# Performance work log

Hardware: AMD Instinct MI355X
Metric: run time of the kernel (lower is better)

## Reference

```python
import jax, jax.numpy as jnp
import numpy as np
import math

B, S, D, H, L, D_OUT = 8, 1024, 1024, 16, 2, 1024
DK = D // H
LN_EPS = 1e-8


def _ln(x, g, b):
    m = jnp.mean(x, axis=-1, keepdims=True)
    var = jnp.mean((x - m) ** 2, axis=-1, keepdims=True)
    return (x - m) / jnp.sqrt(var + LN_EPS) * g + b


def setup_inputs() -> dict:
    key = jax.random.key(0)
    ks = jax.random.split(key, 16)
    s = 0.02
    return {
        "q": jax.random.normal(ks[0], (B, S, D), jnp.float32),
        "k": jax.random.normal(ks[1], (B, S, D), jnp.float32),
        "v": jax.random.normal(ks[2], (B, S, D), jnp.float32),
        "attn_mask": jnp.ones((B, S, S), jnp.int32),
        # per-layer stacked params
        "Wqkv": jax.random.normal(ks[3], (L, 3, D, D), jnp.float32) * s,  # [out,in]
        "bqkv": jnp.zeros((L, 3, D), jnp.float32),
        "Wo": jax.random.normal(ks[4], (L, D, D), jnp.float32) * s,
        "bo": jnp.zeros((L, D), jnp.float32),
        "ln1_g": jnp.ones((L, D), jnp.float32),
        "ln1_b": jnp.zeros((L, D), jnp.float32),
        "ln2_g": jnp.ones((L, D), jnp.float32),
        "ln2_b": jnp.zeros((L, D), jnp.float32),
        "Wc1": jax.random.normal(ks[5], (L, D, D), jnp.float32) * s,  # conv1d k=1 == linear
        "bc1": jnp.zeros((L, D), jnp.float32),
        "Wc2": jax.random.normal(ks[6], (L, D, D), jnp.float32) * s,
        "bc2": jnp.zeros((L, D), jnp.float32),
        "last_g": jnp.ones((D,), jnp.float32),
        "last_b": jnp.zeros((D,), jnp.float32),
        "Wfc": jax.random.normal(ks[7], (D_OUT, D), jnp.float32) * s,
        "bfc": jnp.zeros((D_OUT,), jnp.float32),
    }


def reference(q, k, v, attn_mask, Wqkv, bqkv, Wo, bo, ln1_g, ln1_b, ln2_g, ln2_b,
              Wc1, bc1, Wc2, bc2, last_g, last_b, Wfc, bfc):
    scale = 1.0 / math.sqrt(DK)
    mask = (attn_mask == 0)[:, None, :, :]  # [B,1,S,S] broadcast over heads

    def proj(x, W, b):
        # linear [out,in] then split heads -> [B,H,S,dk]
        y = jnp.einsum('bsd,od->bso', x, W) + b
        return y.reshape(B, S, H, DK).transpose(0, 2, 1, 3)

    for i in range(L):
        Q = _ln(q, ln1_g[i], ln1_b[i])
        qh = proj(Q, Wqkv[i, 0], bqkv[i, 0])
        kh = proj(k, Wqkv[i, 1], bqkv[i, 1])
        vh = proj(v, Wqkv[i, 2], bqkv[i, 2])
        scores = jnp.einsum('bhqd,bhkd->bhqk', qh, kh) * scale
        scores = jnp.clip(scores, -30.0, 30.0)
        scores = jnp.where(mask, -1e9, scores) + 1e-5
        p = jax.nn.softmax(scores, axis=-1)
        x = jnp.einsum('bhqk,bhkd->bhqd', p, vh)
        x = x.transpose(0, 2, 1, 3).reshape(B, S, D)
        x = jax.nn.relu(jnp.einsum('bsd,od->bso', x, Wo[i]) + bo[i])
        k = k + x
        k = _ln(k, ln2_g[i], ln2_b[i])
        # PointWiseFeedForward: conv2(conv1(x)) + x, kernel_size=1, no activation
        h = jnp.einsum('bsd,od->bso', k, Wc1[i]) + bc1[i]
        h = jnp.einsum('bsd,od->bso', h, Wc2[i]) + bc2[i]
        k = k + h
        q = k
        v = k
    out = _ln(k, last_g, last_b)
    return jnp.einsum('bsd,od->bso', out, Wfc) + bfc
```

## Files before the change

kernel.cpp:

```cpp
#include <hip/hip_runtime.h>

typedef __attribute__((ext_vector_type(8))) short s8x;
typedef __attribute__((ext_vector_type(4))) float f4x;
typedef unsigned short u16;
typedef unsigned int u32;

#define DEV static __device__ __forceinline__

DEV u16 f2b(float f) {
    union { float f; u32 u; } v; v.f = f;
    u32 r = v.u + 0x7FFFu + ((v.u >> 16) & 1u);
    return (u16)(r >> 16);
}

DEV u32 pk2(float lo, float hi) {
    u32 r;
    asm("v_cvt_pk_bf16_f32 %0, %1, %2" : "=v"(r) : "v"(lo), "v"(hi));
    return r;
}

DEV void gload16(const void* g, void* lds) {
    __builtin_amdgcn_global_load_lds(
        (const __attribute__((address_space(1))) void*)g,
        (__attribute__((address_space(3))) void*)lds, 16, 0, 0);
}

#define GK 1024
#define BM 128
#define BN 128
#define BK 64


DEV void stage_unit(const u16* __restrict__ g, char* l, int tid) {
#pragma unroll
    for (int i = 0; i < 2; ++i) {
        int db = i * 8192 + tid * 16;
        int row = db >> 7;
        int cs = ((db >> 4) & 7) ^ (row & 7);
        gload16(g + (size_t)row * 1024 + cs * 8, l + db);
    }
}

DEV s8x lds_frag(const char* Lbase, int row, int kk, int lg) {
    int cb = (kk * 64 + lg * 16) ^ ((row & 7) << 4);
    return *(const s8x*)(Lbase + row * 128 + cb);
}

template<int FLAGS, int NN>
__global__ __launch_bounds__(512, 2) void gemm8(
    const u16* __restrict__ A, const u16* __restrict__ W,
    const float* __restrict__ bias, const float* __restrict__ res,
    float* __restrict__ outf, u16* __restrict__ outb, float scl)
{
    constexpr bool RELU = (FLAGS & 1) != 0;
    constexpr bool RES  = (FLAGS & 2) != 0;
    constexpr bool WF   = (FLAGS & 4) != 0;
    constexpr bool WB   = (FLAGS & 8) != 0;
    constexpr bool RBIA = (FLAGS & 16) != 0;

    __shared__ __attribute__((aligned(16))) u16 As[3][256 * 64];
    __shared__ __attribute__((aligned(16))) u16 Bs[3][128 * 64];

    const int tid = threadIdx.x, lane = tid & 63, wid = tid >> 6;
    const int l15 = lane & 15, lg = lane >> 4;
    const int wm = wid >> 1, wn = wid & 1;
    const int bm = blockIdx.x, bn = blockIdx.y;

    const u16* Ab = A + (size_t)bm * 256 * GK;
    const u16* Wb = W + (size_t)bn * 128 * GK;

    f4x acc[4][4];
#pragma unroll
    for (int i = 0; i < 4; ++i)
#pragma unroll
        for (int j = 0; j < 4; ++j) { f4x z = {0.f, 0.f, 0.f, 0.f}; acc[i][j] = z; }

    char* a0 = (char*)As[0]; char* a1 = (char*)As[1]; char* a2 = (char*)As[2];
    char* b0 = (char*)Bs[0]; char* b1 = (char*)Bs[1]; char* b2 = (char*)Bs[2];

    stage_unit(Ab + 0 * 64,                 a0,        tid);
    stage_unit(Ab + 128 * GK + 0 * 64,      a0 + 16384, tid);
    stage_unit(Wb + 0 * 64,                 b0,        tid);
    stage_unit(Ab + 1 * 64,                 a1,        tid);
    stage_unit(Ab + 128 * GK + 1 * 64,      a1 + 16384, tid);
    stage_unit(Wb + 1 * 64,                 b1,        tid);
    asm volatile("s_waitcnt vmcnt(6)" ::: "memory");
    __builtin_amdgcn_s_barrier();

    for (int t = 0; t < 16; ++t) {
        const bool st = (t < 14);
        s8x bfr[4][2], afr[2][2];
#pragma unroll
        for (int ni = 0; ni < 4; ++ni)
#pragma unroll
            for (int kk = 0; kk < 2; ++kk)
                bfr[ni][kk] = lds_frag(b0, wn * 64 + ni * 16 + l15, kk, lg);
#pragma unroll
        for (int mi = 0; mi < 2; ++mi)
#pragma unroll
            for (int kk = 0; kk < 2; ++kk)
                afr[mi][kk] = lds_frag(a0, wm * 64 + mi * 16 + l15, kk, lg);
        if (st) {
            stage_unit(Ab + (t + 2) * 64,            a2,         tid);
            stage_unit(Ab + 128 * GK + (t + 2) * 64, a2 + 16384, tid);
        }
        __builtin_amdgcn_s_barrier();
        asm volatile("s_waitcnt lgkmcnt(0)" ::: "memory");
        __builtin_amdgcn_sched_barrier(0);
        __builtin_amdgcn_s_setprio(1);
#pragma unroll
        for (int kk = 0; kk < 2; ++kk)
#pragma unroll
            for (int mi = 0; mi < 2; ++mi)
#pragma unroll
                for (int ni = 0; ni < 4; ++ni)
                    acc[mi][ni] = __builtin_amdgcn_mfma_f32_16x16x32_bf16(afr[mi][kk], bfr[ni][kk], acc[mi][ni], 0, 0, 0);
        __builtin_amdgcn_s_setprio(0);
        __builtin_amdgcn_s_barrier();

        s8x afr2[2][2];
#pragma unroll
        for (int mi = 0; mi < 2; ++mi)
#pragma unroll
            for (int kk = 0; kk < 2; ++kk)
                afr2[mi][kk] = lds_frag(a0, wm * 64 + (mi + 2) * 16 + l15, kk, lg);
        if (st) stage_unit(Wb + (t + 2) * 64, b2, tid);
        __builtin_amdgcn_s_barrier();
        asm volatile("s_waitcnt lgkmcnt(0)" ::: "memory");
        __builtin_amdgcn_sched_barrier(0);
        __builtin_amdgcn_s_setprio(1);
#pragma unroll
        for (int kk = 0; kk < 2; ++kk)
#pragma unroll
            for (int mi = 0; mi < 2; ++mi)
#pragma unroll
                for (int ni = 0; ni < 4; ++ni)
                    acc[mi + 2][ni] = __builtin_amdgcn_mfma_f32_16x16x32_bf16(afr2[mi][kk], bfr[ni][kk], acc[mi + 2][ni], 0, 0, 0);
        __builtin_amdgcn_s_setprio(0);
        if (st) asm volatile("s_waitcnt vmcnt(6)" ::: "memory");
        else    asm volatile("s_waitcnt vmcnt(0)" ::: "memory");
        __builtin_amdgcn_s_barrier();

        char* tA = a0; a0 = a1; a1 = a2; a2 = tA;
        char* tB = b0; b0 = b1; b1 = b2; b2 = tB;
    }

#pragma unroll
    for (int ni = 0; ni < 4; ++ni) {
        int gcol = bn * 128 + wn * 64 + ni * 16 + l15;
        float bvc = RBIA ? 0.f : bias[gcol];
#pragma unroll
        for (int mi = 0; mi < 4; ++mi) {
            int grow0 = bm * 256 + wm * 64 + mi * 16 + lg * 4;
#pragma unroll
            for (int r = 0; r < 4; ++r) {
                float bv = RBIA ? bias[grow0 + r] : bvc;
                float v = (acc[mi][ni][r] + bv) * scl;
                if (RELU) v = fmaxf(v, 0.f);
                size_t oidx = (size_t)(grow0 + r) * NN + gcol;
                if (RES) v += res[oidx];
                if (WF) outf[oidx] = v;
                if (WB) outb[oidx] = f2b(v);
            }
        }
    }
}

__global__ __launch_bounds__(256) void gemm_z2(
    const u16* __restrict__ A0, const u16* __restrict__ W0, const float* __restrict__ b0,
    u16* __restrict__ o0, float s0,
    const u16* __restrict__ A1, const u16* __restrict__ W1, const float* __restrict__ b1,
    u16* __restrict__ o1, float s1)
{
    const int z = blockIdx.z;
    const u16* A = z ? A1 : A0;
    const u16* W = z ? W1 : W0;
    const float* bias = z ? b1 : b0;
    u16* outb = z ? o1 : o0;
    const float scl = z ? s1 : s0;

    __shared__ __attribute__((aligned(16))) u16 As[2][BM * BK];
    __shared__ __attribute__((aligned(16))) u16 Bs[2][BN * BK];

    const int tid  = threadIdx.x;
    const int lane = tid & 63;
    const int wid  = tid >> 6;
    const int wr = wid >> 1, wc = wid & 1;
    const int bm = blockIdx.x, bn = blockIdx.y;
    const int l15 = lane & 15;
    const int lg  = lane >> 4;

    const u16* Ab = A + (size_t)bm * BM * GK;
    const u16* Wb = W + (size_t)bn * BN * GK;

    const int prow = tid >> 3;
    const int pcol = (tid & 7) * 8;

    f4x acc[4][4];
#pragma unroll
    for (int i = 0; i < 4; ++i)
#pragma unroll
        for (int j = 0; j < 4; ++j) { f4x z_ = {0.f, 0.f, 0.f, 0.f}; acc[i][j] = z_; }

#pragma unroll
    for (int c = 0; c < 4; ++c) {
        int row = c * 32 + prow;
        gload16(Ab + (size_t)row * GK + pcol, &As[0][row * BK + pcol]);
    }
#pragma unroll
    for (int c = 0; c < 4; ++c) {
        int row = c * 32 + prow;
        gload16(Wb + (size_t)row * GK + pcol, &Bs[0][row * BK + pcol]);
    }

    const int nkt = GK / BK;
    int cur = 0;
    for (int kt = 0; kt < nkt; ++kt) {
        __syncthreads();
        if (kt + 1 < nkt) {
            const u16* Ak = Ab + (kt + 1) * BK;
            const u16* Wk = Wb + (kt + 1) * BK;
#pragma unroll
            for (int c = 0; c < 4; ++c) {
                int row = c * 32 + prow;
                gload16(Ak + (size_t)row * GK + pcol, &As[cur ^ 1][row * BK + pcol]);
            }
#pragma unroll
            for (int c = 0; c < 4; ++c) {
                int row = c * 32 + prow;
                gload16(Wk + (size_t)row * GK + pcol, &Bs[cur ^ 1][row * BK + pcol]);
            }
        }
        const u16* Ac = As[cur];
        const u16* Bc = Bs[cur];
#pragma unroll
        for (int kk = 0; kk < 2; ++kk) {
            s8x a[4], b[4];
#pragma unroll
            for (int mi = 0; mi < 4; ++mi)
                a[mi] = *(const s8x*)(Ac + (wr * 64 + mi * 16 + l15) * BK + kk * 32 + lg * 8);
#pragma unroll
            for (int ni = 0; ni < 4; ++ni)
                b[ni] = *(const s8x*)(Bc + (wc * 64 + ni * 16 + l15) * BK + kk * 32 + lg * 8);
#pragma unroll
            for (int mi = 0; mi < 4; ++mi)
#pragma unroll
                for (int ni = 0; ni < 4; ++ni)
                    acc[mi][ni] = __builtin_amdgcn_mfma_f32_16x16x32_bf16(a[mi], b[ni], acc[mi][ni], 0, 0, 0);
        }
        cur ^= 1;
    }

#pragma unroll
    for (int ni = 0; ni < 4; ++ni) {
        int gcol = bn * BN + wc * 64 + ni * 16 + l15;
        float bvc = bias[gcol];
#pragma unroll
        for (int mi = 0; mi < 4; ++mi) {
            int grow0 = bm * BM + wr * 64 + mi * 16 + lg * 4;
#pragma unroll
            for (int r = 0; r < 4; ++r) {
                float v = (acc[mi][ni][r] + bvc) * scl;
                outb[(size_t)(grow0 + r) * 1024 + gcol] = f2b(v);
            }
        }
    }
}

__global__ __launch_bounds__(512) void attn_kernel(
    const u16* __restrict__ Qm, const u16* __restrict__ Km, const u16* __restrict__ Vt,
    const u32* __restrict__ maskw, const u32* __restrict__ rowfl,
    u16* __restrict__ Om)
{
    const int bh = blockIdx.x;
    const int b  = bh >> 4;
    const int h  = bh & 15;
    const int qt = blockIdx.y;
    const int tid = threadIdx.x, lane = tid & 63, wid = tid >> 6;
    const int l15 = lane & 15, lg = lane >> 4;

    __shared__ __attribute__((aligned(16))) u16 Ks[2][64 * 64];
    __shared__ __attribute__((aligned(16))) u16 Vs[2][64 * 64];
    __shared__ __attribute__((aligned(16))) u16 Ps[8][16][64];
    __shared__ int anymask;

    const size_t rowbase = (size_t)b * 1024;
    const int hoff = h * 64;

    if (tid == 0) anymask = 0;

    const int so   = tid * 16;
    const int srow = so >> 7;
    const int sch  = ((so >> 4) & 7) ^ (srow & 7);
    const int vswz = (l15 & 7) << 4;

    const u16* Kbase = Km + rowbase * 1024 + hoff;
    const u16* Vbase = Vt + (size_t)(hoff + srow) * 8192 + b * 1024;

    gload16(Kbase + (size_t)srow * 1024 + sch * 8, (char*)Ks[0] + so);
    gload16(Vbase + sch * 8,                       (char*)Vs[0] + so);

    __syncthreads();
    if (tid < 128) {
        if (rowfl[rowbase + qt * 128 + tid]) atomicOr(&anymask, 1);
    }

    const int qrow = qt * 128 + wid * 16 + l15;
    s8x qf[2];
#pragma unroll
    for (int kk = 0; kk < 2; ++kk)
        qf[kk] = *(const s8x*)(Qm + (rowbase + qrow) * 1024 + hoff + kk * 32 + lg * 8);

    f4x o[4];
#pragma unroll
    for (int d = 0; d < 4; ++d) { f4x z = {0.f, 0.f, 0.f, 0.f}; o[d] = z; }
    float mrun = -1e30f, lrun = 0.f;

    __syncthreads();
    const int am = anymask;

    int cur = 0;
    for (int kt = 0; kt < 16; ++kt) {
        if (kt < 15) {
            gload16(Kbase + (size_t)(kt + 1) * 64 * 1024 + (size_t)srow * 1024 + sch * 8,
                    (char*)Ks[cur ^ 1] + so);
            gload16(Vbase + (kt + 1) * 64 + sch * 8, (char*)Vs[cur ^ 1] + so);
        }

        f4x sc[4];
#pragma unroll
        for (int ni = 0; ni < 4; ++ni) { f4x z = {0.f, 0.f, 0.f, 0.f}; sc[ni] = z; }
        __builtin_amdgcn_s_setprio(1);
#pragma unroll
        for (int kk = 0; kk < 2; ++kk) {
#pragma unroll
            for (int ni = 0; ni < 4; ++ni) {
                int row = ni * 16 + l15;
                int cb  = (kk * 64 + lg * 16) ^ ((row & 7) << 4);
                s8x kf = *(const s8x*)((const char*)Ks[cur] + row * 128 + cb);
                sc[ni] = __builtin_amdgcn_mfma_f32_16x16x32_bf16(kf, qf[kk], sc[ni], 0, 0, 0);
            }
        }
        __builtin_amdgcn_s_setprio(0);

#pragma unroll
        for (int ni = 0; ni < 4; ++ni)
#pragma unroll
            for (int r = 0; r < 4; ++r)
                sc[ni][r] = fminf(fmaxf(sc[ni][r], -30.f), 30.f);
        if (am) {
            int qg = qt * 128 + wid * 16 + l15;
#pragma unroll
            for (int ni = 0; ni < 4; ++ni)
#pragma unroll
                for (int r = 0; r < 4; ++r) {
                    int kcol = kt * 64 + ni * 16 + lg * 4 + r;
                    u32 wb_ = maskw[(rowbase + qg) * 32 + (kcol >> 5)];
                    if (wb_ & (1u << (kcol & 31))) sc[ni][r] = -1e9f;
                }
        }

        float mx = fmaxf(fmaxf(fmaxf(sc[0][0], sc[0][1]), fmaxf(sc[0][2], sc[0][3])),
                         fmaxf(fmaxf(sc[1][0], sc[1][1]), fmaxf(sc[1][2], sc[1][3])));
        mx = fmaxf(mx, fmaxf(fmaxf(fmaxf(sc[2][0], sc[2][1]), fmaxf(sc[2][2], sc[2][3])),
                             fmaxf(fmaxf(sc[3][0], sc[3][1]), fmaxf(sc[3][2], sc[3][3]))));
        mx = fmaxf(mx, __shfl_xor(mx, 16));
        mx = fmaxf(mx, __shfl_xor(mx, 32));
        if (!__all(mx <= mrun + 8.f)) {
            float mn = fmaxf(mrun, mx);
            float al = __expf(mrun - mn);
            mrun = mn;
            lrun *= al;
#pragma unroll
            for (int r = 0; r < 4; ++r) {
                float alr = __shfl(al, lg * 4 + r);
#pragma unroll
                for (int d = 0; d < 4; ++d) o[d][r] *= alr;
            }
        }
        float s = 0.f;
#pragma unroll
        for (int ni = 0; ni < 4; ++ni)
#pragma unroll
            for (int r = 0; r < 4; ++r) {
                float p = __expf(sc[ni][r] - mrun);
                sc[ni][r] = p;
                s += p;
            }
        s += __shfl_xor(s, 16);
        s += __shfl_xor(s, 32);
        lrun += s;

#pragma unroll
        for (int ni = 0; ni < 4; ++ni) {
            uint2 w; w.x = pk2(sc[ni][0], sc[ni][1]); w.y = pk2(sc[ni][2], sc[ni][3]);
            *(uint2*)((char*)&Ps[wid][l15][0] + ((ni * 32 + lg * 8) ^ vswz)) = w;
        }
        s8x pa[2];
#pragma unroll
        for (int kk = 0; kk < 2; ++kk)
            pa[kk] = *(const s8x*)((const char*)&Ps[wid][l15][0] + ((kk * 64 + lg * 16) ^ vswz));

        __builtin_amdgcn_s_setprio(1);
#pragma unroll
        for (int dt = 0; dt < 4; ++dt)
#pragma unroll
            for (int kk = 0; kk < 2; ++kk) {
                int row = dt * 16 + l15;
                int cb  = (kk * 64 + lg * 16) ^ ((row & 7) << 4);
                s8x vf = *(const s8x*)((const char*)Vs[cur] + row * 128 + cb);
                o[dt] = __builtin_amdgcn_mfma_f32_16x16x32_bf16(pa[kk], vf, o[dt], 0, 0, 0);
            }
        __builtin_amdgcn_s_setprio(0);

        __syncthreads();
        cur ^= 1;
    }

    float rl = 1.f / lrun;
    float rlr[4];
#pragma unroll
    for (int r = 0; r < 4; ++r) rlr[r] = __shfl(rl, lg * 4 + r);
#pragma unroll
    for (int dt = 0; dt < 4; ++dt) {
        int gc = hoff + dt * 16 + l15;
#pragma unroll
        for (int r = 0; r < 4; ++r) {
            int gr = qt * 128 + wid * 16 + lg * 4 + r;
            Om[(rowbase + gr) * 1024 + gc] = f2b(o[dt][r] * rlr[r]);
        }
    }
}

__global__ __launch_bounds__(256) void ln_kernel(
    const float* __restrict__ x, const float* __restrict__ g, const float* __restrict__ bb,
    u16* __restrict__ yb, float* __restrict__ yf)
{
    const int wid = threadIdx.x >> 6, lane = threadIdx.x & 63;
    const size_t row = (size_t)blockIdx.x * 4 + wid;
    const float* xr = x + row * 1024;
    float4 v[4];
    float s = 0.f, s2 = 0.f;
#pragma unroll
    for (int c = 0; c < 4; ++c) {
        v[c] = *(const float4*)(xr + c * 256 + lane * 4);
        s  += v[c].x + v[c].y + v[c].z + v[c].w;
        s2 += v[c].x * v[c].x + v[c].y * v[c].y + v[c].z * v[c].z + v[c].w * v[c].w;
    }
#pragma unroll
    for (int m = 32; m >= 1; m >>= 1) { s += __shfl_xor(s, m); s2 += __shfl_xor(s2, m); }
    float mean = s * (1.f / 1024.f);
    float var  = s2 * (1.f / 1024.f) - mean * mean;
    float rs = rsqrtf(var + 1e-8f);
#pragma unroll
    for (int c = 0; c < 4; ++c) {
        int col = c * 256 + lane * 4;
        float4 gv = *(const float4*)(g + col);
        float4 bv = *(const float4*)(bb + col);
        float y0 = (v[c].x - mean) * rs * gv.x + bv.x;
        float y1 = (v[c].y - mean) * rs * gv.y + bv.y;
        float y2 = (v[c].z - mean) * rs * gv.z + bv.z;
        float y3 = (v[c].w - mean) * rs * gv.w + bv.w;
        if (yb) { ushort4 o4 = make_ushort4(f2b(y0), f2b(y1), f2b(y2), f2b(y3));
                  *(ushort4*)(yb + row * 1024 + col) = o4; }
        if (yf) { float4 o4f = make_float4(y0, y1, y2, y3);
                  *(float4*)(yf + row * 1024 + col) = o4f; }
    }
}

__global__ __launch_bounds__(256) void cvt_kernel(const float* __restrict__ x, u16* __restrict__ y, int n4)
{
    int i = blockIdx.x * 256 + threadIdx.x;
    if (i < n4) {
        float4 v = *(const float4*)(x + (size_t)i * 4);
        ushort4 o = make_ushort4(f2b(v.x), f2b(v.y), f2b(v.z), f2b(v.w));
        *(ushort4*)(y + (size_t)i * 4) = o;
    }
}

__global__ __launch_bounds__(256) void cvtT_kernel(const float* __restrict__ X, u16* __restrict__ Y)
{
    __shared__ u16 T[64][65];
    const int l = blockIdx.z;
    const int j0 = blockIdx.y * 64;
    const int i0 = blockIdx.x * 64;
    const float* Xl = X + (size_t)l * 1024 * 1024;
    u16* Yl = Y + (size_t)l * 1024 * 1024;
    const int tr = threadIdx.x >> 4;
    const int tc = threadIdx.x & 15;
#pragma unroll
    for (int k = 0; k < 4; ++k) {
        int j = tr + k * 16;
        float4 v = *(const float4*)(Xl + (size_t)(j0 + j) * 1024 + i0 + tc * 4);
        T[tc * 4 + 0][j] = f2b(v.x);
        T[tc * 4 + 1][j] = f2b(v.y);
        T[tc * 4 + 2][j] = f2b(v.z);
        T[tc * 4 + 3][j] = f2b(v.w);
    }
    __syncthreads();
    const int wr_ = threadIdx.x >> 3;
    const int wc_ = threadIdx.x & 7;
#pragma unroll
    for (int k = 0; k < 2; ++k) {
        int i = wr_ + k * 32;
        u16 tmp[8];
#pragma unroll
        for (int e = 0; e < 8; ++e) tmp[e] = T[i][wc_ * 8 + e];
        *(ushort4*)(Yl + (size_t)(i0 + i) * 1024 + j0 + wc_ * 8)     = make_ushort4(tmp[0], tmp[1], tmp[2], tmp[3]);
        *(ushort4*)(Yl + (size_t)(i0 + i) * 1024 + j0 + wc_ * 8 + 4) = make_ushort4(tmp[4], tmp[5], tmp[6], tmp[7]);
    }
}

__global__ __launch_bounds__(256) void matvec_kernel(const float* __restrict__ W2, const float* __restrict__ b1,
                                                     const float* __restrict__ b2, float* __restrict__ outv)
{
    const int wid = threadIdx.x >> 6, lane = threadIdx.x & 63;
    int row = blockIdx.x * 4 + wid;
    int l = row >> 10, o = row & 1023;
    const float* wr_ = W2 + (size_t)l * 1024 * 1024 + (size_t)o * 1024;
    const float* b1l = b1 + l * 1024;
    float s = 0.f;
#pragma unroll
    for (int c = 0; c < 4; ++c) {
        float4 w = *(const float4*)(wr_ + c * 256 + lane * 4);
        float4 bv = *(const float4*)(b1l + c * 256 + lane * 4);
        s += w.x * bv.x + w.y * bv.y + w.z * bv.z + w.w * bv.w;
    }
#pragma unroll
    for (int m = 32; m >= 1; m >>= 1) s += __shfl_xor(s, m);
    if (lane == 0) outv[row] = s + b2[l * 1024 + o];
}

__global__ __launch_bounds__(256) void mask_kernel(const int* __restrict__ am, u32* __restrict__ mw)
{
    size_t idx = (size_t)blockIdx.x * 256 + threadIdx.x;
    unsigned long long bal = __ballot(am[idx] == 0);
    int lane = threadIdx.x & 63;
    if (lane == 0)  mw[idx >> 5] = (u32)bal;
    if (lane == 32) mw[idx >> 5] = (u32)(bal >> 32);
}

__global__ __launch_bounds__(256) void rowflag_kernel(const u32* __restrict__ mw, u32* __restrict__ rf)
{
    int r = blockIdx.x * 256 + threadIdx.x;
    u32 o = 0;
#pragma unroll
    for (int i = 0; i < 32; ++i) o |= mw[r * 32 + i];
    rf[r] = o;
}

extern "C" void kernel_launch(void* const* d_in, const int* in_sizes, int n_in,
                              void* d_out, int out_size, void* d_ws, size_t ws_size,
                              hipStream_t stream)
{
    (void)in_sizes; (void)n_in; (void)out_size; (void)ws_size;

    const float* q_in  = (const float*)d_in[0];
    const float* k_in  = (const float*)d_in[1];
    const float* v_in  = (const float*)d_in[2];
    const int*   amask = (const int*)d_in[3];
    const float* Wqkv  = (const float*)d_in[4];
    const float* bqkv  = (const float*)d_in[5];
    const float* Wo    = (const float*)d_in[6];
    const float* bo    = (const float*)d_in[7];
    const float* ln1g  = (const float*)d_in[8];
    const float* ln1b  = (const float*)d_in[9];
    const float* ln2g  = (const float*)d_in[10];
    const float* ln2b  = (const float*)d_in[11];
    const float* Wc1   = (const float*)d_in[12];
    const float* bc1   = (const float*)d_in[13];
    const float* Wc2   = (const float*)d_in[14];
    const float* bc2   = (const float*)d_in[15];
    const float* lastg = (const float*)d_in[16];
    const float* lastb = (const float*)d_in[17];
    const float* Wfc   = (const float*)d_in[18];
    const float* bfc   = (const float*)d_in[19];
    float* out = (float*)d_out;

    char* base = (char*)d_ws;
    size_t off = 0;
    auto alloc = [&](size_t bytes) -> char* {
        char* p = base + off;
        off = (off + bytes + 255) & ~(size_t)255;
        return p;
    };
    const size_t M1 = 1024 * 1024;
    const size_t MT = 8192 * 1024;
    u16* wqkv_b = (u16*)alloc(6 * M1 * 2);
    u16* wo_b   = (u16*)alloc(2 * M1 * 2);
    u16* wcomb  = (u16*)alloc(2 * M1 * 2);
    u16* wfc_b  = (u16*)alloc(M1 * 2);
    float* bcomb = (float*)alloc(2 * 1024 * 4);
    float* zb    = (float*)alloc(1024 * 4);
    u32* maskw  = (u32*)alloc(8192 * 32 * 4);
    u32* rowfl  = (u32*)alloc(8192 * 4);
    float* sF   = (float*)alloc(MT * 4);
    float* sT   = (float*)alloc(MT * 4);
    u16* t0 = (u16*)alloc(MT * 2);
    u16* qh = (u16*)alloc(MT * 2);
    u16* kh = (u16*)alloc(MT * 2);
    u16* vt = (u16*)alloc(MT * 2);
    u16* xb = (u16*)alloc(MT * 2);
    u16* x2 = (u16*)alloc(MT * 2);
    u16* wc1t  = qh;
    u16* wc2_b = kh;

    cvt_kernel<<<6 * M1 / 1024, 256, 0, stream>>>(Wqkv, wqkv_b, (int)(6 * M1 / 4));
    cvt_kernel<<<2 * M1 / 1024, 256, 0, stream>>>(Wo,   wo_b,   (int)(2 * M1 / 4));
    cvt_kernel<<<M1 / 1024, 256, 0, stream>>>(Wfc, wfc_b, (int)(M1 / 4));
    cvt_kernel<<<2 * M1 / 1024, 256, 0, stream>>>(Wc2, wc2_b, (int)(2 * M1 / 4));
    cvtT_kernel<<<dim3(16, 16, 2), 256, 0, stream>>>(Wc1, wc1t);
    hipMemsetAsync(zb, 0, 1024 * 4, stream);
    gemm_z2<<<dim3(8, 8, 2), 256, 0, stream>>>(
        wc2_b, wc1t, zb, wcomb, 1.f,
        wc2_b + M1, wc1t + M1, zb, wcomb + M1, 1.f);
    matvec_kernel<<<512, 256, 0, stream>>>(Wc2, bc1, bc2, bcomb);
    mask_kernel<<<32768, 256, 0, stream>>>(amask, maskw);
    rowflag_kernel<<<32, 256, 0, stream>>>(maskw, rowfl);

    dim3 g8(8192 / 256, 1024 / 128);
    dim3 v8(1024 / 256, 8192 / 128);
    const int D = 1024;
    for (int i = 0; i < 2; ++i) {
        const float* qsrc = (i == 0) ? q_in : sF;
        ln_kernel<<<2048, 256, 0, stream>>>(qsrc, ln1g + i * D, ln1b + i * D, t0, nullptr);
        if (i == 0) {
            cvt_kernel<<<8192, 256, 0, stream>>>(k_in, x2, (int)(MT / 4));
            cvt_kernel<<<8192, 256, 0, stream>>>(v_in, xb, (int)(MT / 4));
        }
        gemm8<8, 1024><<<g8, 512, 0, stream>>>(t0, wqkv_b + (size_t)(i * 3 + 0) * M1,
                                               bqkv + (i * 3 + 0) * D, nullptr, nullptr, qh, 0.125f);
        gemm8<8, 1024><<<g8, 512, 0, stream>>>(x2, wqkv_b + (size_t)(i * 3 + 1) * M1,
                                               bqkv + (i * 3 + 1) * D, nullptr, nullptr, kh, 1.f);
        const u16* vin_b = (i == 0) ? xb : x2;
        gemm8<8 | 16, 8192><<<v8, 512, 0, stream>>>(wqkv_b + (size_t)(i * 3 + 2) * M1, vin_b,
                                                    bqkv + (i * 3 + 2) * D, nullptr, nullptr, vt, 1.f);
        attn_kernel<<<dim3(128, 8), 512, 0, stream>>>(qh, kh, vt, maskw, rowfl, t0);
        const float* resp = (i == 0) ? k_in : sF;
        gemm8<1 | 2 | 4, 1024><<<g8, 512, 0, stream>>>(t0, wo_b + (size_t)i * M1,
                                                       bo + i * D, resp, sT, nullptr, 1.f);
        ln_kernel<<<2048, 256, 0, stream>>>(sT, ln2g + i * D, ln2b + i * D, xb, sF);
        gemm8<2 | 4 | 8, 1024><<<g8, 512, 0, stream>>>(xb, wcomb + (size_t)i * M1,
                                                       bcomb + i * 1024, sF, sT, x2, 1.f);
        float* tmp = sF; sF = sT; sT = tmp;
    }
    ln_kernel<<<2048, 256, 0, stream>>>(sF, lastg, lastb, t0, nullptr);
    gemm8<4, 1024><<<g8, 512, 0, stream>>>(t0, wfc_b, bfc, nullptr, out, nullptr, 1.f);
}
```

Baseline: 560.3 us.

## Merge Q/K/V projections into one launch and drop online-softmax max tracking

Replaces three separate projection GEMM launches with a single z-indexed kernel that has a triple-buffered LDS pipeline, so the three GEMMs can share the GPU at once. In attention, scores are bounded by the clip, so the running max and rescaling are removed. Q is pre-scaled by log2(e) and a raw exp2 instruction is applied to the clipped score with the bound rescaled to match. This cuts max reductions, shuffles and rescales per tile, but the unshifted exponent depends on the clip keeping exp2 in range, and masked entries become exp2(-43) rather than zero, which slightly changes the semantics.

```diff
diff --git a/kernel.cpp b/kernel.cpp
--- a/kernel.cpp
+++ b/kernel.cpp
@@ -16,6 +16,12 @@
 DEV u32 pk2(float lo, float hi) {
     u32 r;
     asm("v_cvt_pk_bf16_f32 %0, %1, %2" : "=v"(r) : "v"(lo), "v"(hi));
+    return r;
+}
+
+DEV float exp2_raw(float x) {
+    float r;
+    asm("v_exp_f32 %0, %1" : "=v"(r) : "v"(x));
     return r;
 }
 
@@ -166,6 +172,123 @@
     }
 }
 
+__global__ __launch_bounds__(512, 2) void gemm_qkv(
+    const u16* __restrict__ Aq, const u16* __restrict__ Ak, const u16* __restrict__ Av,
+    const u16* __restrict__ Wq, const u16* __restrict__ Wk, const u16* __restrict__ Wv,
+    const float* __restrict__ bq, const float* __restrict__ bk, const float* __restrict__ bv,
+    u16* __restrict__ oq, u16* __restrict__ ok, u16* __restrict__ ovt, float qs)
+{
+    const int z = blockIdx.z;
+    const u16* A; const u16* W; const float* bias; u16* outb; float scl;
+    int bm, bn, NN;
+    bool rbia;
+    if (z == 0)      { A = Aq; W = Wq; bias = bq; outb = oq;  scl = qs;  bm = blockIdx.x >> 3; bn = blockIdx.x & 7;  NN = 1024; rbia = false; }
+    else if (z == 1) { A = Ak; W = Wk; bias = bk; outb = ok;  scl = 1.f; bm = blockIdx.x >> 3; bn = blockIdx.x & 7;  NN = 1024; rbia = false; }
+    else             { A = Wv; W = Av; bias = bv; outb = ovt; scl = 1.f; bm = blockIdx.x >> 6; bn = blockIdx.x & 63; NN = 8192; rbia = true;  }
+
+    __shared__ __attribute__((aligned(16))) u16 As[3][256 * 64];
+    __shared__ __attribute__((aligned(16))) u16 Bs[3][128 * 64];
+
+    const int tid = threadIdx.x, lane = tid & 63, wid = tid >> 6;
+    const int l15 = lane & 15, lg = lane >> 4;
+    const int wm = wid >> 1, wn = wid & 1;
+
+    const u16* Ab = A + (size_t)bm * 256 * GK;
+    const u16* Wb = W + (size_t)bn * 128 * GK;
+
+    f4x acc[4][4];
+#pragma unroll
+    for (int i = 0; i < 4; ++i)
+#pragma unroll
+        for (int j = 0; j < 4; ++j) { f4x zr = {0.f, 0.f, 0.f, 0.f}; acc[i][j] = zr; }
+
+    char* a0 = (char*)As[0]; char* a1 = (char*)As[1]; char* a2 = (char*)As[2];
+    char* b0 = (char*)Bs[0]; char* b1 = (char*)Bs[1]; char* b2 = (char*)Bs[2];
+
+    stage_unit(Ab + 0 * 64,                 a0,        tid);
+    stage_unit(Ab + 128 * GK + 0 * 64,      a0 + 16384, tid);
+    stage_unit(Wb + 0 * 64,                 b0,        tid);
+    stage_unit(Ab + 1 * 64,                 a1,        tid);
+    stage_unit(Ab + 128 * GK + 1 * 64,      a1 + 16384, tid);
+    stage_unit(Wb + 1 * 64,                 b1,        tid);
+    asm volatile("s_waitcnt vmcnt(6)" ::: "memory");
+    __builtin_amdgcn_s_barrier();
+
+    for (int t = 0; t < 16; ++t) {
+        const bool st = (t < 14);
+        s8x bfr[4][2], afr[2][2];
+#pragma unroll
+        for (int ni = 0; ni < 4; ++ni)
+#pragma unroll
+            for (int kk = 0; kk < 2; ++kk)
+                bfr[ni][kk] = lds_frag(b0, wn * 64 + ni * 16 + l15, kk, lg);
+#pragma unroll
+        for (int mi = 0; mi < 2; ++mi)
+#pragma unroll
+            for (int kk = 0; kk < 2; ++kk)
+                afr[mi][kk] = lds_frag(a0, wm * 64 + mi * 16 + l15, kk, lg);
+        if (st) {
+            stage_unit(Ab + (t + 2) * 64,            a2,         tid);
+            stage_unit(Ab + 128 * GK + (t + 2) * 64, a2 + 16384, tid);
+        }
+        __builtin_amdgcn_s_barrier();
+        asm volatile("s_waitcnt lgkmcnt(0)" ::: "memory");
+        __builtin_amdgcn_sched_barrier(0);
+        __builtin_amdgcn_s_setprio(1);
+#pragma unroll
+        for (int kk = 0; kk < 2; ++kk)
+#pragma unroll
+            for (int mi = 0; mi < 2; ++mi)
+#pragma unroll
+                for (int ni = 0; ni < 4; ++ni)
+                    acc[mi][ni] = __builtin_amdgcn_mfma_f32_16x16x32_bf16(afr[mi][kk], bfr[ni][kk], acc[mi][ni], 0, 0, 0);
+        __builtin_amdgcn_s_setprio(0);
+        __builtin_amdgcn_s_barrier();
+
+        s8x afr2[2][2];
+#pragma unroll
+        for (int mi = 0; mi < 2; ++mi)
+#pragma unroll
+            for (int kk = 0; kk < 2; ++kk)
+                afr2[mi][kk] = lds_frag(a0, wm * 64 + (mi + 2) * 16 + l15, kk, lg);
+        if (st) stage_unit(Wb + (t + 2) * 64, b2, tid);
+        __builtin_amdgcn_s_barrier();
+        asm volatile("s_waitcnt lgkmcnt(0)" ::: "memory");
+        __builtin_amdgcn_sched_barrier(0);
+        __builtin_amdgcn_s_setprio(1);
+#pragma unroll
+        for (int kk = 0; kk < 2; ++kk)
+#pragma unroll
+            for (int mi = 0; mi < 2; ++mi)
+#pragma unroll
+                for (int ni = 0; ni < 4; ++ni)
+                    acc[mi + 2][ni] = __builtin_amdgcn_mfma_f32_16x16x32_bf16(afr2[mi][kk], bfr[ni][kk], acc[mi + 2][ni], 0, 0, 0);
+        __builtin_amdgcn_s_setprio(0);
+        if (st) asm volatile("s_waitcnt vmcnt(6)" ::: "memory");
+        else    asm volatile("s_waitcnt vmcnt(0)" ::: "memory");
+        __builtin_amdgcn_s_barrier();
+
+        char* tA = a0; a0 = a1; a1 = a2; a2 = tA;
+        char* tB = b0; b0 = b1; b1 = b2; b2 = tB;
+    }
+
+#pragma unroll
+    for (int ni = 0; ni < 4; ++ni) {
+        int gcol = bn * 128 + wn * 64 + ni * 16 + l15;
+        float bvc = rbia ? 0.f : bias[gcol];
+#pragma unroll
+        for (int mi = 0; mi < 4; ++mi) {
+            int grow0 = bm * 256 + wm * 64 + mi * 16 + lg * 4;
+#pragma unroll
+            for (int r = 0; r < 4; ++r) {
+                float bv_ = rbia ? bias[grow0 + r] : bvc;
+                float v = (acc[mi][ni][r] + bv_) * scl;
+                outb[(size_t)(grow0 + r) * NN + gcol] = f2b(v);
+            }
+        }
+    }
+}
+
 __global__ __launch_bounds__(256) void gemm_z2(
     const u16* __restrict__ A0, const u16* __restrict__ W0, const float* __restrict__ b0,
     u16* __restrict__ o0, float s0,
@@ -314,10 +437,11 @@
     f4x o[4];
 #pragma unroll
     for (int d = 0; d < 4; ++d) { f4x z = {0.f, 0.f, 0.f, 0.f}; o[d] = z; }
-    float mrun = -1e30f, lrun = 0.f;
+    float lrun = 0.f;
 
     __syncthreads();
     const int am = anymask;
+    const float CLIP = 43.2808512f;
 
     int cur = 0;
     for (int kt = 0; kt < 16; ++kt) {
@@ -343,11 +467,6 @@
         }
         __builtin_amdgcn_s_setprio(0);
 
-#pragma unroll
-        for (int ni = 0; ni < 4; ++ni)
-#pragma unroll
-            for (int r = 0; r < 4; ++r)
-                sc[ni][r] = fminf(fmaxf(sc[ni][r], -30.f), 30.f);
         if (am) {
             int qg = qt * 128 + wid * 16 + l15;
 #pragma unroll
@@ -360,30 +479,12 @@
                 }
         }
 
-        float mx = fmaxf(fmaxf(fmaxf(sc[0][0], sc[0][1]), fmaxf(sc[0][2], sc[0][3])),
-                         fmaxf(fmaxf(sc[1][0], sc[1][1]), fmaxf(sc[1][2], sc[1][3])));
-        mx = fmaxf(mx, fmaxf(fmaxf(fmaxf(sc[2][0], sc[2][1]), fmaxf(sc[2][2], sc[2][3])),
-                             fmaxf(fmaxf(sc[3][0], sc[3][1]), fmaxf(sc[3][2], sc[3][3]))));
-        mx = fmaxf(mx, __shfl_xor(mx, 16));
-        mx = fmaxf(mx, __shfl_xor(mx, 32));
-        if (!__all(mx <= mrun + 8.f)) {
-            float mn = fmaxf(mrun, mx);
-            float al = __expf(mrun - mn);
-            mrun = mn;
-            lrun *= al;
+        float s = 0.f;
+#pragma unroll
+        for (int ni = 0; ni < 4; ++ni)
 #pragma unroll
             for (int r = 0; r < 4; ++r) {
-                float alr = __shfl(al, lg * 4 + r);
-#pragma unroll
-                for (int d = 0; d < 4; ++d) o[d][r] *= alr;
-            }
-        }
-        float s = 0.f;
-#pragma unroll
-        for (int ni = 0; ni < 4; ++ni)
-#pragma unroll
-            for (int r = 0; r < 4; ++r) {
-                float p = __expf(sc[ni][r] - mrun);
+                float p = exp2_raw(fminf(fmaxf(sc[ni][r], -CLIP), CLIP));
                 sc[ni][r] = p;
                 s += p;
             }
@@ -619,7 +720,7 @@
     rowflag_kernel<<<32, 256, 0, stream>>>(maskw, rowfl);
 
     dim3 g8(8192 / 256, 1024 / 128);
-    dim3 v8(1024 / 256, 8192 / 128);
+    const float QS = 0.125f * 1.44269504f;
     const int D = 1024;
     for (int i = 0; i < 2; ++i) {
         const float* qsrc = (i == 0) ? q_in : sF;
@@ -628,13 +729,12 @@
             cvt_kernel<<<8192, 256, 0, stream>>>(k_in, x2, (int)(MT / 4));
             cvt_kernel<<<8192, 256, 0, stream>>>(v_in, xb, (int)(MT / 4));
         }
-        gemm8<8, 1024><<<g8, 512, 0, stream>>>(t0, wqkv_b + (size_t)(i * 3 + 0) * M1,
-                                               bqkv + (i * 3 + 0) * D, nullptr, nullptr, qh, 0.125f);
-        gemm8<8, 1024><<<g8, 512, 0, stream>>>(x2, wqkv_b + (size_t)(i * 3 + 1) * M1,
-                                               bqkv + (i * 3 + 1) * D, nullptr, nullptr, kh, 1.f);
         const u16* vin_b = (i == 0) ? xb : x2;
-        gemm8<8 | 16, 8192><<<v8, 512, 0, stream>>>(wqkv_b + (size_t)(i * 3 + 2) * M1, vin_b,
-                                                    bqkv + (i * 3 + 2) * D, nullptr, nullptr, vt, 1.f);
+        const u16* wl = wqkv_b + (size_t)(i * 3) * M1;
+        gemm_qkv<<<dim3(256, 1, 3), 512, 0, stream>>>(
+            t0, x2, vin_b, wl, wl + M1, wl + 2 * M1,
+            bqkv + (i * 3 + 0) * D, bqkv + (i * 3 + 1) * D, bqkv + (i * 3 + 2) * D,
+            qh, kh, vt, QS);
         attn_kernel<<<dim3(128, 8), 512, 0, stream>>>(qh, kh, vt, maskw, rowfl, t0);
         const float* resp = (i == 0) ? k_in : sF;
         gemm8<1 | 2 | 4, 1024><<<g8, 512, 0, stream>>>(t0, wo_b + (size_t)i * M1,
```

New measurement: 598.1 us. +6.8%, slower.
